# Optimization experiments

Measured on AMD Instinct MI355X. Metric: run time of the kernel, lower is better.

The kernel has to match this reference:

```python
import jax, jax.numpy as jnp
import numpy as np

COMMITMENT = 0.25
EPS = 1e-10


def setup_inputs() -> dict:
    key = jax.random.key(0)
    k1, k2 = jax.random.split(key)
    x = jax.random.normal(k1, (16, 16384, 64), dtype=jnp.float32)
    embed = jax.random.normal(k2, (64, 512), dtype=jnp.float32)  # [embed_dim, n_embed]
    sigma = jnp.ones((1,), dtype=jnp.float32)
    return {"x": x, "embed": embed, "sigma": sigma}


def reference(x, embed, sigma):
    # x: [B, T, D]; embed: [D, K]; sigma: [1]
    D, K = embed.shape
    flat = x.reshape(-1, D)  # [N, D]
    dist = (jnp.sum(flat * flat, axis=1, keepdims=True)
            - 2.0 * (flat @ embed)
            + jnp.sum(embed * embed, axis=0, keepdims=True))
    soft_assign = jax.nn.softmax(-sigma * dist, axis=1)  # [N, K]
    likelihoods = jnp.mean(soft_assign, axis=0)          # [K]
    embed_ind = jnp.argmax(soft_assign, axis=1)          # [N]
    hard = jnp.take(embed.T, embed_ind, axis=0)          # [N, D] gather of codewords
    soft_proj = soft_assign @ embed.T                    # [N, D]
    # straight-through: forward = hard, backward = soft path
    quantize = (soft_proj + jax.lax.stop_gradient(hard - soft_proj)).reshape(x.shape)
    # KL(uniform || likelihoods.detach()), batchmean over K, scaled by commitment
    p = 1.0 / K
    ql = jax.lax.stop_gradient(likelihoods)
    quant_loss = COMMITMENT * jnp.mean(p * (jnp.log(p) - jnp.log(ql + EPS)))
    return quantize, quant_loss, likelihoods
```

## Files before the change

kernel.cpp:

```cpp
#include <hip/hip_runtime.h>

#define NROWS    262144
#define DIMS     64
#define KCODES   512
#define MTILE    32
#define RPW      4
#define CHUNK    256
#define NCHUNK   2
#define D_PER    16
#define D_CHUNKS 4
#define NTHREADS 512

typedef int v8i __attribute__((ext_vector_type(8)));

__device__ __forceinline__ float dpp_xor1(float v) {
    int i = __builtin_amdgcn_update_dpp(0, __float_as_int(v), 0xB1, 0xF, 0xF, true);
    return __int_as_float(i);
}
__device__ __forceinline__ float dpp_xor2(float v) {
    int i = __builtin_amdgcn_update_dpp(0, __float_as_int(v), 0x4E, 0xF, 0xF, true);
    return __int_as_float(i);
}

__global__ void prep_kernel(const float* __restrict__ embed,
                            float* __restrict__ embedT,
                            float* __restrict__ enorm,
                            float* __restrict__ lik) {
    int k = blockIdx.x;
    int d = threadIdx.x;
    float v = embed[d * KCODES + k];
    embedT[k * DIMS + d] = v;
    float sq = __fmul_rn(v, v);
    int j = d & 7;
    float r = __shfl(sq, j, 64);
#pragma unroll
    for (int i = 1; i < 8; ++i)
        r = __fadd_rn(r, __shfl(sq, j + 8 * i, 64));
    float t;
    t = __shfl_xor(r, 1, 64); r = __fadd_rn(r, t);
    t = __shfl_xor(r, 2, 64); r = __fadd_rn(r, t);
    t = __shfl_xor(r, 4, 64); r = __fadd_rn(r, t);
    if (d == 0) { enorm[k] = r; lik[k] = 0.0f; }
}

__launch_bounds__(NTHREADS)
__global__ void main_kernel(const float* __restrict__ x,
                            const float* __restrict__ embed,
                            const float* __restrict__ sigma,
                            const float* __restrict__ embedT,
                            const float* __restrict__ enorm,
                            float* __restrict__ lik,
                            float* __restrict__ out) {
    __shared__ float e_lds[D_PER * KCODES];

    const int tid = threadIdx.x;
    const int cg  = tid & 63;
    const int rg  = tid >> 6;
    const int rowbase = blockIdx.x * MTILE + rg * RPW;

    const float sigma_v = sigma[0];

    float acc[NCHUNK][RPW][4];
#pragma unroll
    for (int c = 0; c < NCHUNK; ++c)
#pragma unroll
        for (int r = 0; r < RPW; ++r)
#pragma unroll
            for (int q = 0; q < 4; ++q) acc[c][r][q] = 0.0f;

    const float4* __restrict__ eg4 = reinterpret_cast<const float4*>(embed);
    float4* e_lds4 = reinterpret_cast<float4*>(e_lds);

    const int rg_s = __builtin_amdgcn_readfirstlane(rg);
    const float* xwave = x + (size_t)(blockIdx.x * MTILE + rg_s * RPW) * DIMS;

    for (int dc = 0; dc < D_CHUNKS; ++dc) {
        __syncthreads();
#pragma unroll
        for (int i = 0; i < 4; ++i) {
            int f4 = tid + i * NTHREADS;
            e_lds4[f4] = eg4[dc * (D_PER * KCODES / 4) + f4];
        }
        __syncthreads();

        const float4* e4 = reinterpret_cast<const float4*>(e_lds);

#pragma unroll
        for (int ph = 0; ph < 2; ++ph) {
            const float* p0 = xwave + 0 * DIMS + dc * D_PER + ph * 8;
            const float* p1 = xwave + 1 * DIMS + dc * D_PER + ph * 8;
            const float* p2 = xwave + 2 * DIMS + dc * D_PER + ph * 8;
            const float* p3 = xwave + 3 * DIMS + dc * D_PER + ph * 8;
            v8i xs0, xs1, xs2, xs3;
            asm volatile("s_load_dwordx8 %0, %4, 0\n\t"
                         "s_load_dwordx8 %1, %5, 0\n\t"
                         "s_load_dwordx8 %2, %6, 0\n\t"
                         "s_load_dwordx8 %3, %7, 0\n\t"
                         "s_waitcnt lgkmcnt(0)"
                         : "=&s"(xs0), "=&s"(xs1), "=&s"(xs2), "=&s"(xs3)
                         : "s"(p0), "s"(p1), "s"(p2), "s"(p3));

#pragma unroll
            for (int d2l = 0; d2l < 4; ++d2l) {
                const int d2 = ph * 4 + d2l;
                float4 e0a = e4[(2 * d2 + 0) * 128 +  0 + cg];
                float4 e1a = e4[(2 * d2 + 1) * 128 +  0 + cg];
                float4 e0b = e4[(2 * d2 + 0) * 128 + 64 + cg];
                float4 e1b = e4[(2 * d2 + 1) * 128 + 64 + cg];

#define ROW_FMA(r, xs)                                                        \
                {                                                             \
                    float xlo = __int_as_float(xs[2 * d2l]);                  \
                    float xhi = __int_as_float(xs[2 * d2l + 1]);              \
                    acc[0][r][0] = fmaf(xlo, e0a.x, acc[0][r][0]);            \
                    acc[0][r][1] = fmaf(xlo, e0a.y, acc[0][r][1]);            \
                    acc[0][r][2] = fmaf(xlo, e0a.z, acc[0][r][2]);            \
                    acc[0][r][3] = fmaf(xlo, e0a.w, acc[0][r][3]);            \
                    acc[0][r][0] = fmaf(xhi, e1a.x, acc[0][r][0]);            \
                    acc[0][r][1] = fmaf(xhi, e1a.y, acc[0][r][1]);            \
                    acc[0][r][2] = fmaf(xhi, e1a.z, acc[0][r][2]);            \
                    acc[0][r][3] = fmaf(xhi, e1a.w, acc[0][r][3]);            \
                    acc[1][r][0] = fmaf(xlo, e0b.x, acc[1][r][0]);            \
                    acc[1][r][1] = fmaf(xlo, e0b.y, acc[1][r][1]);            \
                    acc[1][r][2] = fmaf(xlo, e0b.z, acc[1][r][2]);            \
                    acc[1][r][3] = fmaf(xlo, e0b.w, acc[1][r][3]);            \
                    acc[1][r][0] = fmaf(xhi, e1b.x, acc[1][r][0]);            \
                    acc[1][r][1] = fmaf(xhi, e1b.y, acc[1][r][1]);            \
                    acc[1][r][2] = fmaf(xhi, e1b.z, acc[1][r][2]);            \
                    acc[1][r][3] = fmaf(xhi, e1b.w, acc[1][r][3]);            \
                }
                ROW_FMA(0, xs0)
                ROW_FMA(1, xs1)
                ROW_FMA(2, xs2)
                ROW_FMA(3, xs3)
#undef ROW_FMA
            }
        }
    }

    const int r_l = (cg >> 3) & 3;
    const int j_l = cg & 7;
    float xr;
    {
        const float* xp = x + (size_t)(rowbase + r_l) * DIMS + j_l;
        float v0 = xp[0];
        float s = __fmul_rn(v0, v0);
#pragma unroll
        for (int i = 1; i < 8; ++i) {
            float v = xp[8 * i];
            s = __fadd_rn(s, __fmul_rn(v, v));
        }
        xr = s;
    }
    {
        float t;
        t = dpp_xor1(xr);          xr = __fadd_rn(xr, t);
        t = dpp_xor2(xr);          xr = __fadd_rn(xr, t);
        t = __shfl_xor(xr, 4, 64); xr = __fadd_rn(xr, t);
    }

    float en[NCHUNK][4];
#pragma unroll
    for (int c = 0; c < NCHUNK; ++c)
#pragma unroll
        for (int q = 0; q < 4; ++q)
            en[c][q] = enorm[c * CHUNK + cg * 4 + q];

    float likpart[NCHUNK][4];
#pragma unroll
    for (int c = 0; c < NCHUNK; ++c)
#pragma unroll
        for (int q = 0; q < 4; ++q) likpart[c][q] = 0.0f;

#pragma unroll
    for (int r = 0; r < RPW; ++r) {
        float xn = __shfl(xr, r * 8, 64);
        float m = -INFINITY;
#pragma unroll
        for (int c = 0; c < NCHUNK; ++c)
#pragma unroll
            for (int q = 0; q < 4; ++q) {
                float dot  = acc[c][r][q];
                float td   = __fsub_rn(xn, __fmul_rn(2.0f, dot));
                float dist = __fadd_rn(td, en[c][q]);
                float zz   = __fmul_rn(-sigma_v, dist);
                acc[c][r][q] = zz;
                m = fmaxf(m, zz);
            }
        m = fmaxf(m, dpp_xor1(m));
        m = fmaxf(m, dpp_xor2(m));
        m = fmaxf(m, __shfl_xor(m,  4, 64));
        m = fmaxf(m, __shfl_xor(m,  8, 64));
        m = fmaxf(m, __shfl_xor(m, 16, 64));
        m = fmaxf(m, __shfl_xor(m, 32, 64));

        float s = 0.0f;
        int lcol = 1024;
#pragma unroll
        for (int c = 0; c < NCHUNK; ++c)
#pragma unroll
            for (int q = 0; q < 4; ++q) {
                float ee = expf(__fsub_rn(acc[c][r][q], m));
                acc[c][r][q] = ee;
                s += ee;
                int col = c * CHUNK + cg * 4 + q;
                lcol = (ee == 1.0f) ? min(lcol, col) : lcol;
            }
        unsigned long long b0 = __ballot(lcol < CHUNK);
        unsigned long long ba = __ballot(lcol < 1024);
        int srcl = (int)(b0 ? __ffsll(b0) : __ffsll(ba)) - 1;
        int bc = __shfl(lcol, srcl, 64);

        s = __fadd_rn(s, dpp_xor1(s));
        s = __fadd_rn(s, dpp_xor2(s));
        s = __fadd_rn(s, __shfl_xor(s,  4, 64));
        s = __fadd_rn(s, __shfl_xor(s,  8, 64));
        s = __fadd_rn(s, __shfl_xor(s, 16, 64));
        s = __fadd_rn(s, __shfl_xor(s, 32, 64));

        float invS = 1.0f / s;
#pragma unroll
        for (int c = 0; c < NCHUNK; ++c)
#pragma unroll
            for (int q = 0; q < 4; ++q)
                likpart[c][q] = fmaf(acc[c][r][q], invS, likpart[c][q]);

        int row = rowbase + r;
        __builtin_nontemporal_store(embedT[bc * DIMS + cg],
                                    &out[(size_t)row * DIMS + cg]);
    }

    float* red = e_lds;
    __syncthreads();
    red[tid] = 0.0f;
    __syncthreads();
#pragma unroll
    for (int c = 0; c < NCHUNK; ++c)
#pragma unroll
        for (int q = 0; q < 4; ++q)
            atomicAdd(&red[c * CHUNK + cg * 4 + q], likpart[c][q]);
    __syncthreads();
    atomicAdd(&lik[tid], red[tid]);
}

__global__ void finish_kernel(const float* __restrict__ lik,
                              float* __restrict__ out) {
    int tid = threadIdx.x;
    float l = lik[tid] / 262144.0f;
    out[16777217 + tid] = l;
    const float p = 1.0f / 512.0f;
    float term = __fmul_rn(p, __fsub_rn(logf(p), logf(l + 1e-10f)));
#pragma unroll
    for (int mask = 1; mask < 64; mask <<= 1)
        term += __shfl_xor(term, mask, 64);
    __shared__ float ws[8];
    if ((tid & 63) == 0) ws[tid >> 6] = term;
    __syncthreads();
    if (tid == 0) {
        float ssum = 0.0f;
        for (int i = 0; i < 8; ++i) ssum += ws[i];
        out[16777216] = 0.25f * (ssum / 512.0f);
    }
}

extern "C" void kernel_launch(void* const* d_in, const int* in_sizes, int n_in,
                              void* d_out, int out_size, void* d_ws, size_t ws_size,
                              hipStream_t stream) {
    const float* x     = (const float*)d_in[0];
    const float* embed = (const float*)d_in[1];
    const float* sigma = (const float*)d_in[2];
    float* out = (float*)d_out;
    float* ws  = (float*)d_ws;

    float* embedT = ws;
    float* enorm  = ws + 32768;
    float* lik    = ws + 33280;

    prep_kernel<<<KCODES, DIMS, 0, stream>>>(embed, embedT, enorm, lik);
    main_kernel<<<NROWS / MTILE, NTHREADS, 0, stream>>>(x, embed, sigma,
                                                        embedT, enorm, lik, out);
    finish_kernel<<<1, NTHREADS, 0, stream>>>(lik, out);
}
```

Baseline: 506.3 us.

## Prefetch next embed chunk into registers and batch scalar x loads

```diff
diff --git a/kernel.cpp b/kernel.cpp
--- a/kernel.cpp
+++ b/kernel.cpp
@@ -9,6 +9,7 @@
 #define NCHUNK   2
 #define D_PER    16
 #define D_CHUNKS 4
+#define STG4     (D_PER * KCODES / 4)
 #define NTHREADS 512
 
 typedef int v8i __attribute__((ext_vector_type(8)));
@@ -74,68 +75,85 @@
     const int rg_s = __builtin_amdgcn_readfirstlane(rg);
     const float* xwave = x + (size_t)(blockIdx.x * MTILE + rg_s * RPW) * DIMS;
 
+    float4 pf0 = eg4[tid];
+    float4 pf1 = eg4[tid + NTHREADS];
+    float4 pf2 = eg4[tid + 2 * NTHREADS];
+    float4 pf3 = eg4[tid + 3 * NTHREADS];
+
     for (int dc = 0; dc < D_CHUNKS; ++dc) {
-        __syncthreads();
-#pragma unroll
-        for (int i = 0; i < 4; ++i) {
-            int f4 = tid + i * NTHREADS;
-            e_lds4[f4] = eg4[dc * (D_PER * KCODES / 4) + f4];
+        const float* px = xwave + dc * D_PER;
+        v8i xs0, xs1, xs2, xs3, ys0, ys1, ys2, ys3;
+        asm volatile("s_load_dwordx8 %0, %8, 0\n\t"
+                     "s_load_dwordx8 %1, %8, 256\n\t"
+                     "s_load_dwordx8 %2, %8, 512\n\t"
+                     "s_load_dwordx8 %3, %8, 768\n\t"
+                     "s_load_dwordx8 %4, %8, 32\n\t"
+                     "s_load_dwordx8 %5, %8, 288\n\t"
+                     "s_load_dwordx8 %6, %8, 544\n\t"
+                     "s_load_dwordx8 %7, %8, 800"
+                     : "=&s"(xs0), "=&s"(xs1), "=&s"(xs2), "=&s"(xs3),
+                       "=&s"(ys0), "=&s"(ys1), "=&s"(ys2), "=&s"(ys3)
+                     : "s"(px));
+
+        __builtin_amdgcn_s_barrier();
+
+        e_lds4[tid]                = pf0;
+        e_lds4[tid + NTHREADS]     = pf1;
+        e_lds4[tid + 2 * NTHREADS] = pf2;
+        e_lds4[tid + 3 * NTHREADS] = pf3;
+
+        if (dc + 1 < D_CHUNKS) {
+            const float4* nx = eg4 + (size_t)(dc + 1) * STG4;
+            pf0 = nx[tid];
+            pf1 = nx[tid + NTHREADS];
+            pf2 = nx[tid + 2 * NTHREADS];
+            pf3 = nx[tid + 3 * NTHREADS];
         }
-        __syncthreads();
+
+        asm volatile("s_waitcnt lgkmcnt(0)" ::: "memory");
+        __builtin_amdgcn_s_barrier();
+
+        asm volatile("s_waitcnt lgkmcnt(0)"
+                     : "+s"(xs0), "+s"(xs1), "+s"(xs2), "+s"(xs3),
+                       "+s"(ys0), "+s"(ys1), "+s"(ys2), "+s"(ys3));
 
         const float4* e4 = reinterpret_cast<const float4*>(e_lds);
 
-#pragma unroll
-        for (int ph = 0; ph < 2; ++ph) {
-            const float* p0 = xwave + 0 * DIMS + dc * D_PER + ph * 8;
-            const float* p1 = xwave + 1 * DIMS + dc * D_PER + ph * 8;
-            const float* p2 = xwave + 2 * DIMS + dc * D_PER + ph * 8;
-            const float* p3 = xwave + 3 * DIMS + dc * D_PER + ph * 8;
-            v8i xs0, xs1, xs2, xs3;
-            asm volatile("s_load_dwordx8 %0, %4, 0\n\t"
-                         "s_load_dwordx8 %1, %5, 0\n\t"
-                         "s_load_dwordx8 %2, %6, 0\n\t"
-                         "s_load_dwordx8 %3, %7, 0\n\t"
-                         "s_waitcnt lgkmcnt(0)"
-                         : "=&s"(xs0), "=&s"(xs1), "=&s"(xs2), "=&s"(xs3)
-                         : "s"(p0), "s"(p1), "s"(p2), "s"(p3));
-
-#pragma unroll
-            for (int d2l = 0; d2l < 4; ++d2l) {
-                const int d2 = ph * 4 + d2l;
-                float4 e0a = e4[(2 * d2 + 0) * 128 +  0 + cg];
-                float4 e1a = e4[(2 * d2 + 1) * 128 +  0 + cg];
-                float4 e0b = e4[(2 * d2 + 0) * 128 + 64 + cg];
-                float4 e1b = e4[(2 * d2 + 1) * 128 + 64 + cg];
-
+#define PHASE(XA, XB, XC, XD, PH)                                             \
+        _Pragma("unroll")                                                     \
+        for (int d2l = 0; d2l < 4; ++d2l) {                                   \
+            const int d2 = (PH) * 4 + d2l;                                    \
+            float4 e0a = e4[(2 * d2 + 0) * 128 +  0 + cg];                    \
+            float4 e1a = e4[(2 * d2 + 1) * 128 +  0 + cg];                    \
+            float4 e0b = e4[(2 * d2 + 0) * 128 + 64 + cg];                    \
+            float4 e1b = e4[(2 * d2 + 1) * 128 + 64 + cg];                    \
+            ROW_FMA(0, XA) ROW_FMA(1, XB) ROW_FMA(2, XC) ROW_FMA(3, XD)       \
+        }
 #define ROW_FMA(r, xs)                                                        \
-                {                                                             \
-                    float xlo = __int_as_float(xs[2 * d2l]);                  \
-                    float xhi = __int_as_float(xs[2 * d2l + 1]);              \
-                    acc[0][r][0] = fmaf(xlo, e0a.x, acc[0][r][0]);            \
-                    acc[0][r][1] = fmaf(xlo, e0a.y, acc[0][r][1]);            \
-                    acc[0][r][2] = fmaf(xlo, e0a.z, acc[0][r][2]);            \
-                    acc[0][r][3] = fmaf(xlo, e0a.w, acc[0][r][3]);            \
-                    acc[0][r][0] = fmaf(xhi, e1a.x, acc[0][r][0]);            \
-                    acc[0][r][1] = fmaf(xhi, e1a.y, acc[0][r][1]);            \
-                    acc[0][r][2] = fmaf(xhi, e1a.z, acc[0][r][2]);            \
-                    acc[0][r][3] = fmaf(xhi, e1a.w, acc[0][r][3]);            \
-                    acc[1][r][0] = fmaf(xlo, e0b.x, acc[1][r][0]);            \
-                    acc[1][r][1] = fmaf(xlo, e0b.y, acc[1][r][1]);            \
-                    acc[1][r][2] = fmaf(xlo, e0b.z, acc[1][r][2]);            \
-                    acc[1][r][3] = fmaf(xlo, e0b.w, acc[1][r][3]);            \
-                    acc[1][r][0] = fmaf(xhi, e1b.x, acc[1][r][0]);            \
-                    acc[1][r][1] = fmaf(xhi, e1b.y, acc[1][r][1]);            \
-                    acc[1][r][2] = fmaf(xhi, e1b.z, acc[1][r][2]);            \
-                    acc[1][r][3] = fmaf(xhi, e1b.w, acc[1][r][3]);            \
-                }
-                ROW_FMA(0, xs0)
-                ROW_FMA(1, xs1)
-                ROW_FMA(2, xs2)
-                ROW_FMA(3, xs3)
+            {                                                                 \
+                float xlo = __int_as_float(xs[2 * d2l]);                      \
+                float xhi = __int_as_float(xs[2 * d2l + 1]);                  \
+                acc[0][r][0] = fmaf(xlo, e0a.x, acc[0][r][0]);                \
+                acc[0][r][1] = fmaf(xlo, e0a.y, acc[0][r][1]);                \
+                acc[0][r][2] = fmaf(xlo, e0a.z, acc[0][r][2]);                \
+                acc[0][r][3] = fmaf(xlo, e0a.w, acc[0][r][3]);                \
+                acc[0][r][0] = fmaf(xhi, e1a.x, acc[0][r][0]);                \
+                acc[0][r][1] = fmaf(xhi, e1a.y, acc[0][r][1]);                \
+                acc[0][r][2] = fmaf(xhi, e1a.z, acc[0][r][2]);                \
+                acc[0][r][3] = fmaf(xhi, e1a.w, acc[0][r][3]);                \
+                acc[1][r][0] = fmaf(xlo, e0b.x, acc[1][r][0]);                \
+                acc[1][r][1] = fmaf(xlo, e0b.y, acc[1][r][1]);                \
+                acc[1][r][2] = fmaf(xlo, e0b.z, acc[1][r][2]);                \
+                acc[1][r][3] = fmaf(xlo, e0b.w, acc[1][r][3]);                \
+                acc[1][r][0] = fmaf(xhi, e1b.x, acc[1][r][0]);                \
+                acc[1][r][1] = fmaf(xhi, e1b.y, acc[1][r][1]);                \
+                acc[1][r][2] = fmaf(xhi, e1b.z, acc[1][r][2]);                \
+                acc[1][r][3] = fmaf(xhi, e1b.w, acc[1][r][3]);                \
+            }
+        PHASE(xs0, xs1, xs2, xs3, 0)
+        PHASE(ys0, ys1, ys2, ys3, 1)
 #undef ROW_FMA
-            }
-        }
+#undef PHASE
     }
 
     const int r_l = (cg >> 3) & 3;
```

After: 554.3 us. 9.5% more time.
